# Kernel tuning notes

Hardware: AMD Instinct MI355X
Metric: run time of the kernel (lower is better)

## Reference

```python
import jax, jax.numpy as jnp
import numpy as np

HIDDEN = 32
N_STEPS = 64  # fixed-step RK4 replaces adaptive Dopri5 (same MLP-eval structure)
STD = 0.1     # init_params: Linear weights ~ N(0, 0.1), biases = 0


def _mlp(w1, b1, w2, b2, w3, b3, y):
    # NODE.forward: fc1 -> relu -> fc2 -> relu -> fc3 (t is unused in the source)
    h = jax.nn.relu(y @ w1 + b1)
    h = jax.nn.relu(h @ w2 + b2)
    return h @ w3 + b3


def setup_inputs() -> dict:
    key = jax.random.key(0)
    ks = jax.random.split(key, 8)
    B, D = 131072, 3
    x = jax.random.normal(ks[0], (B, D), dtype=jnp.float32)
    # eval times in (0.1, 1.0], sorted like a posterior-sample schedule
    samples = jnp.sort(
        jax.random.uniform(ks[1], (8, 1), jnp.float32, 0.1, 1.0), axis=0)
    w1 = (STD * jax.random.normal(ks[2], (D, HIDDEN))).astype(jnp.float32)
    b1 = jnp.zeros((HIDDEN,), jnp.float32)
    w2 = (STD * jax.random.normal(ks[3], (HIDDEN, HIDDEN))).astype(jnp.float32)
    b2 = jnp.zeros((HIDDEN,), jnp.float32)
    w3 = (STD * jax.random.normal(ks[4], (HIDDEN, D))).astype(jnp.float32)
    b3 = jnp.zeros((D,), jnp.float32)
    w_out = (STD * jax.random.normal(ks[5], (D, 1))).astype(jnp.float32)
    b_out = jnp.zeros((1,), jnp.float32)
    return {"x": x, "samples": samples, "w1": w1, "b1": b1, "w2": w2,
            "b2": b2, "w3": w3, "b3": b3, "w_out": w_out, "b_out": b_out}


def reference(x, samples, w1, b1, w2, b2, w3, b3, w_out, b_out):
    t_eval = samples[:, 0]                     # (S,)
    max_T = jnp.max(t_eval)
    dt = max_T / N_STEPS

    def step(y, _):
        k1 = _mlp(w1, b1, w2, b2, w3, b3, y)
        k2 = _mlp(w1, b1, w2, b2, w3, b3, y + 0.5 * dt * k1)
        k3 = _mlp(w1, b1, w2, b2, w3, b3, y + 0.5 * dt * k2)
        k4 = _mlp(w1, b1, w2, b2, w3, b3, y + dt * k3)
        y_new = y + (dt / 6.0) * (k1 + 2.0 * k2 + 2.0 * k3 + k4)
        return y_new, y_new

    # traj[i] is the state at time (i+1)*dt; shape (N_STEPS, B, 3)
    _, traj = jax.lax.scan(jax.checkpoint(step), x, jnp.arange(N_STEPS))

    # gather states at the grid step nearest each eval time
    idx = jnp.clip(jnp.round(t_eval / dt).astype(jnp.int32) - 1, 0, N_STEPS - 1)
    y_eval = traj[idx]                         # (S, B, 3)

    # fc_layers readout -> act_vec (S, B, 1)
    return y_eval @ w_out + b_out
```

## Files before the change

kernel.cpp:

```cpp
#include <hip/hip_runtime.h>

#define NSTEPS 64

typedef __attribute__((ext_vector_type(16))) float float16_;
typedef __attribute__((ext_vector_type(2))) __fp16 half2_;
typedef __attribute__((ext_vector_type(8))) __fp16 half8_;

__device__ __forceinline__ half2_ relu_pk_f16(float a, float b) {
    half2_ h = __builtin_amdgcn_cvt_pkrtz(a, b);
    return __builtin_elementwise_max(h, (half2_)(__fp16)0);
}

__global__ __launch_bounds__(256, 4)
void ode_rk4_mfma(const float* __restrict__ x,
                  const float* __restrict__ samples,
                  const float* __restrict__ w1, const float* __restrict__ b1,
                  const float* __restrict__ w2, const float* __restrict__ b2,
                  const float* __restrict__ w3, const float* __restrict__ b3,
                  const float* __restrict__ w_out, const float* __restrict__ b_out,
                  float* __restrict__ out, int B)
{
    const int lane  = threadIdx.x & 63;
    const int w     = threadIdx.x >> 6;
    const int col32 = lane & 31;
    const int half  = lane >> 5;

    const int rowBase = (blockIdx.x * 4 + w) * 32;
    const int row = rowBase + col32;

    auto pi = [](int m) -> int {
        int bb = (m >> 2) & 3;
        return m + ((bb == 1) ? 4 : (bb == 2) ? -4 : 0);
    };

    union { half2_ h2[4]; half8_ h8; } A1;
    {
        int pm = pi(col32);
        if (half == 0) {
            A1.h2[0] = (half2_){(__fp16)w1[0 * 32 + pm], (__fp16)w1[1 * 32 + pm]};
            A1.h2[1] = (half2_){(__fp16)w1[2 * 32 + pm], (__fp16)b1[pm]};
        } else {
            A1.h2[0] = (half2_)(__fp16)0.0f;
            A1.h2[1] = (half2_)(__fp16)0.0f;
        }
        A1.h2[2] = (half2_)(__fp16)0.0f;
        A1.h2[3] = (half2_)(__fp16)0.0f;
    }

    union { half2_ h2[4]; half8_ h8; } W2T1, W2T2;
#pragma unroll
    for (int pp = 0; pp < 4; ++pp) {
        int i1 = half * 8 + 2 * pp;
        W2T1.h2[pp] = (half2_){(__fp16)w2[i1 * 32 + col32], (__fp16)w2[(i1 + 1) * 32 + col32]};
        W2T2.h2[pp] = (half2_){(__fp16)w2[(i1 + 16) * 32 + col32], (__fp16)w2[(i1 + 17) * 32 + col32]};
    }
    float16_ Cb;
#pragma unroll
    for (int r = 0; r < 16; ++r)
        Cb[r] = b2[(r & 3) + 8 * (r >> 2) + 4 * half];

    union { half2_ h2[4]; half8_ h8; } A31, A32;
    {
        const bool live = (col32 < 8) && ((col32 & 3) < 3);
        const int  d    = col32 & 3;
#pragma unroll
        for (int pp = 0; pp < 4; ++pp) {
            int j0 = 2 * pp;
            int nu0 = 4 * half + (j0 & 3) + 8 * (j0 >> 2);
            if (live) {
                A31.h2[pp] = (half2_){(__fp16)w3[nu0 * 3 + d], (__fp16)w3[(nu0 + 1) * 3 + d]};
                A32.h2[pp] = (half2_){(__fp16)w3[(nu0 + 16) * 3 + d], (__fp16)w3[(nu0 + 17) * 3 + d]};
            } else {
                A31.h2[pp] = (half2_)(__fp16)0.0f;
                A32.h2[pp] = (half2_)(__fp16)0.0f;
            }
        }
    }

    float16_ Zc;
#pragma unroll
    for (int r = 0; r < 16; ++r) Zc[r] = 0.0f;

    const float maxT = samples[7];
    const float dt   = maxT / 64.0f;
    const float dt2  = 0.5f * dt;
    const float dt6  = dt / 6.0f;

    int sidx[8];
    unsigned long long smask = 0ull;
#pragma unroll
    for (int j = 0; j < 8; ++j) {
        int id = (int)rintf(samples[j] / dt) - 1;
        id = id < 0 ? 0 : (id > NSTEPS - 1 ? NSTEPS - 1 : id);
        id = __builtin_amdgcn_readfirstlane(id);
        sidx[j] = id;
        smask |= 1ull << id;
    }
    const float wo0 = w_out[0], wo1 = w_out[1], wo2 = w_out[2];
    const float bo  = b_out[0];
    const float b30 = b3[0], b31 = b3[1], b32 = b3[2];

    float y0 = x[(size_t)row * 3 + 0];
    float y1 = x[(size_t)row * 3 + 1];
    float y2 = x[(size_t)row * 3 + 2];

#pragma unroll 1
    for (int s = 0; s < NSTEPS; ++s) {
        float acc0 = 0.f, acc1 = 0.f, acc2 = 0.f;
        float a0 = y0, a1 = y1, a2 = y2;

#pragma unroll
        for (int st = 0; st < 4; ++st) {
            half2_ a01 = __builtin_amdgcn_cvt_pkrtz(a0, a1);
            half2_ a2o = __builtin_amdgcn_cvt_pkrtz(a2, 1.0f);
            union { half2_ h2[4]; half8_ h8; } BL1;
            BL1.h2[0] = a01; BL1.h2[1] = a2o;
            BL1.h2[2] = a01; BL1.h2[3] = a2o;

            float16_ D1 = __builtin_amdgcn_mfma_f32_32x32x16_f16(A1.h8, BL1.h8, Zc, 0, 0, 0);

            union { half2_ h2[4]; half8_ h8; } B1, B2;
#pragma unroll
            for (int pp = 0; pp < 4; ++pp) {
                B1.h2[pp] = relu_pk_f16(D1[2 * pp], D1[2 * pp + 1]);
                B2.h2[pp] = relu_pk_f16(D1[8 + 2 * pp], D1[8 + 2 * pp + 1]);
            }

            float16_ D2a = __builtin_amdgcn_mfma_f32_32x32x16_f16(W2T1.h8, B1.h8, Cb, 0, 0, 0);
            float16_ D2b = __builtin_amdgcn_mfma_f32_32x32x16_f16(W2T2.h8, B2.h8, Zc, 0, 0, 0);

            union { half2_ h2[4]; half8_ h8; } H1, H2;
#pragma unroll
            for (int pp = 0; pp < 4; ++pp) {
                H1.h2[pp] = relu_pk_f16(D2a[2 * pp] + D2b[2 * pp],
                                        D2a[2 * pp + 1] + D2b[2 * pp + 1]);
                H2.h2[pp] = relu_pk_f16(D2a[8 + 2 * pp] + D2b[8 + 2 * pp],
                                        D2a[8 + 2 * pp + 1] + D2b[8 + 2 * pp + 1]);
            }

            float16_ D3a = __builtin_amdgcn_mfma_f32_32x32x16_f16(A31.h8, H1.h8, Zc, 0, 0, 0);
            float16_ D3b = __builtin_amdgcn_mfma_f32_32x32x16_f16(A32.h8, H2.h8, Zc, 0, 0, 0);

            float k0 = D3a[0] + D3b[0] + b30;
            float k1 = D3a[1] + D3b[1] + b31;
            float k2 = D3a[2] + D3b[2] + b32;

            const float ca = (st == 1 || st == 2) ? 2.0f : 1.0f;
            acc0 = fmaf(ca, k0, acc0); acc1 = fmaf(ca, k1, acc1); acc2 = fmaf(ca, k2, acc2);
            const float ci = (st == 2) ? dt : dt2;
            a0 = fmaf(ci, k0, y0); a1 = fmaf(ci, k1, y1); a2 = fmaf(ci, k2, y2);
        }
        y0 = fmaf(dt6, acc0, y0); y1 = fmaf(dt6, acc1, y1); y2 = fmaf(dt6, acc2, y2);

        if ((smask >> s) & 1ull) {
            if (half == 0) {
#pragma unroll
                for (int j = 0; j < 8; ++j) {
                    if (sidx[j] == s) {
                        out[(size_t)j * B + row] = fmaf(y2, wo2, fmaf(y1, wo1, fmaf(y0, wo0, bo)));
                    }
                }
            }
        }
    }
}

extern "C" void kernel_launch(void* const* d_in, const int* in_sizes, int n_in,
                              void* d_out, int out_size, void* d_ws, size_t ws_size,
                              hipStream_t stream) {
    const float* x       = (const float*)d_in[0];
    const float* samples = (const float*)d_in[1];
    const float* w1      = (const float*)d_in[2];
    const float* b1      = (const float*)d_in[3];
    const float* w2      = (const float*)d_in[4];
    const float* b2      = (const float*)d_in[5];
    const float* w3      = (const float*)d_in[6];
    const float* b3      = (const float*)d_in[7];
    const float* w_out   = (const float*)d_in[8];
    const float* b_out   = (const float*)d_in[9];
    float* out = (float*)d_out;

    const int B = in_sizes[0] / 3;
    const int rowsPerBlock = 128;
    const int grid = (B + rowsPerBlock - 1) / rowsPerBlock;
    ode_rk4_mfma<<<grid, 256, 0, stream>>>(
        x, samples, w1, b1, w2, b2, w3, b3, w_out, b_out, out, B);
}
```

Baseline: 227.2 us.

## Fold fc3 into fc1 and carry RK4 state in hidden pre-activation space

Uses linearity to compose W3 with W1 into a 32x32 matrix, so each RK stage needs only the fc2 MMAs plus one fused fc1 update, and the 3-dim state is never rebuilt inside the step. The layer-2 activations are summed in fp16 (SSl/SSh), and the output state is rebuilt only at sample steps via W3 plus a closed-form bias term. This cuts per-step MFMA and conversion work. In exchange, accumulating the trajectory in fp16 over 64 steps risks drift and precision loss.

Result: faster. 207.2 us (-8.8%).

```diff
diff --git a/kernel.cpp b/kernel.cpp
--- a/kernel.cpp
+++ b/kernel.cpp
@@ -3,15 +3,15 @@
 #define NSTEPS 64
 
 typedef __attribute__((ext_vector_type(16))) float float16_;
-typedef __attribute__((ext_vector_type(2))) __fp16 half2_;
-typedef __attribute__((ext_vector_type(8))) __fp16 half8_;
+typedef __attribute__((ext_vector_type(2)))  __fp16 half2_;
+typedef __attribute__((ext_vector_type(8)))  __fp16 half8_;
 
 __device__ __forceinline__ half2_ relu_pk_f16(float a, float b) {
     half2_ h = __builtin_amdgcn_cvt_pkrtz(a, b);
     return __builtin_elementwise_max(h, (half2_)(__fp16)0);
 }
 
-__global__ __launch_bounds__(256, 4)
+__global__ __launch_bounds__(256, 3)
 void ode_rk4_mfma(const float* __restrict__ x,
                   const float* __restrict__ samples,
                   const float* __restrict__ w1, const float* __restrict__ b1,
@@ -25,66 +25,70 @@
     const int col32 = lane & 31;
     const int half  = lane >> 5;
 
-    const int rowBase = (blockIdx.x * 4 + w) * 32;
-    const int row = rowBase + col32;
-
-    auto pi = [](int m) -> int {
-        int bb = (m >> 2) & 3;
-        return m + ((bb == 1) ? 4 : (bb == 2) ? -4 : 0);
+    const int row = (blockIdx.x * 4 + w) * 32 + col32;
+
+    auto nu = [](int k) -> int {
+        return 16 * (k >> 4) + 4 * ((k >> 3) & 1) + (k & 3) + 8 * (((k & 7)) >> 2);
     };
-
-    union { half2_ h2[4]; half8_ h8; } A1;
-    {
-        int pm = pi(col32);
-        if (half == 0) {
-            A1.h2[0] = (half2_){(__fp16)w1[0 * 32 + pm], (__fp16)w1[1 * 32 + pm]};
-            A1.h2[1] = (half2_){(__fp16)w1[2 * 32 + pm], (__fp16)b1[pm]};
-        } else {
-            A1.h2[0] = (half2_)(__fp16)0.0f;
-            A1.h2[1] = (half2_)(__fp16)0.0f;
-        }
-        A1.h2[2] = (half2_)(__fp16)0.0f;
-        A1.h2[3] = (half2_)(__fp16)0.0f;
-    }
-
-    union { half2_ h2[4]; half8_ h8; } W2T1, W2T2;
-#pragma unroll
-    for (int pp = 0; pp < 4; ++pp) {
-        int i1 = half * 8 + 2 * pp;
-        W2T1.h2[pp] = (half2_){(__fp16)w2[i1 * 32 + col32], (__fp16)w2[(i1 + 1) * 32 + col32]};
-        W2T2.h2[pp] = (half2_){(__fp16)w2[(i1 + 16) * 32 + col32], (__fp16)w2[(i1 + 17) * 32 + col32]};
-    }
-    float16_ Cb;
-#pragma unroll
-    for (int r = 0; r < 16; ++r)
-        Cb[r] = b2[(r & 3) + 8 * (r >> 2) + 4 * half];
-
-    union { half2_ h2[4]; half8_ h8; } A31, A32;
-    {
-        const bool live = (col32 < 8) && ((col32 & 3) < 3);
-        const int  d    = col32 & 3;
-#pragma unroll
-        for (int pp = 0; pp < 4; ++pp) {
-            int j0 = 2 * pp;
-            int nu0 = 4 * half + (j0 & 3) + 8 * (j0 >> 2);
-            if (live) {
-                A31.h2[pp] = (half2_){(__fp16)w3[nu0 * 3 + d], (__fp16)w3[(nu0 + 1) * 3 + d]};
-                A32.h2[pp] = (half2_){(__fp16)w3[(nu0 + 16) * 3 + d], (__fp16)w3[(nu0 + 17) * 3 + d]};
-            } else {
-                A31.h2[pp] = (half2_)(__fp16)0.0f;
-                A32.h2[pp] = (half2_)(__fp16)0.0f;
-            }
-        }
-    }
-
-    float16_ Zc;
-#pragma unroll
-    for (int r = 0; r < 16; ++r) Zc[r] = 0.0f;
+    auto rpos = [&](int t) -> int { return (t & 3) + 8 * (t >> 2) + 4 * half; };
 
     const float maxT = samples[7];
     const float dt   = maxT / 64.0f;
     const float dt2  = 0.5f * dt;
     const float dt6  = dt / 6.0f;
+
+    union F { half2_ h2[4]; half8_ h8; };
+
+    F Mh1, Mh2, Mz1, Mz2;
+#pragma unroll
+    for (int pp = 0; pp < 4; ++pp) {
+        int j0 = 2 * pp;
+        int iA = nu(8 * half + j0),      iB = nu(8 * half + j0 + 1);
+        int iC = nu(16 + 8 * half + j0), iD = nu(16 + 8 * half + j0 + 1);
+        float mA = w3[iA * 3 + 0] * w1[0 * 32 + col32] + w3[iA * 3 + 1] * w1[1 * 32 + col32] + w3[iA * 3 + 2] * w1[2 * 32 + col32];
+        float mB = w3[iB * 3 + 0] * w1[0 * 32 + col32] + w3[iB * 3 + 1] * w1[1 * 32 + col32] + w3[iB * 3 + 2] * w1[2 * 32 + col32];
+        float mC = w3[iC * 3 + 0] * w1[0 * 32 + col32] + w3[iC * 3 + 1] * w1[1 * 32 + col32] + w3[iC * 3 + 2] * w1[2 * 32 + col32];
+        float mD = w3[iD * 3 + 0] * w1[0 * 32 + col32] + w3[iD * 3 + 1] * w1[1 * 32 + col32] + w3[iD * 3 + 2] * w1[2 * 32 + col32];
+        Mh1.h2[pp] = (half2_){(__fp16)(dt2 * mA), (__fp16)(dt2 * mB)};
+        Mh2.h2[pp] = (half2_){(__fp16)(dt2 * mC), (__fp16)(dt2 * mD)};
+        Mz1.h2[pp] = (half2_){(__fp16)(dt6 * mA), (__fp16)(dt6 * mB)};
+        Mz2.h2[pp] = (half2_){(__fp16)(dt6 * mC), (__fp16)(dt6 * mD)};
+    }
+
+    F W2T1, W2T2;
+#pragma unroll
+    for (int pp = 0; pp < 4; ++pp) {
+        int j0 = 2 * pp;
+        int iA = nu(8 * half + j0),      iB = nu(8 * half + j0 + 1);
+        int iC = nu(16 + 8 * half + j0), iD = nu(16 + 8 * half + j0 + 1);
+        W2T1.h2[pp] = (half2_){(__fp16)w2[iA * 32 + col32], (__fp16)w2[iB * 32 + col32]};
+        W2T2.h2[pp] = (half2_){(__fp16)w2[iC * 32 + col32], (__fp16)w2[iD * 32 + col32]};
+    }
+    float16_ Cb;
+#pragma unroll
+    for (int r = 0; r < 16; ++r)
+        Cb[r] = b2[rpos(r)];
+
+    F A31, A32;
+    {
+        const int  d    = col32 & 3;
+        const bool live = (col32 < 8) && (d < 3);
+#pragma unroll
+        for (int pp = 0; pp < 4; ++pp) {
+            int j0 = 2 * pp;
+            int iA = nu(8 * half + j0),      iB = nu(8 * half + j0 + 1);
+            int iC = nu(16 + 8 * half + j0), iD = nu(16 + 8 * half + j0 + 1);
+            A31.h2[pp] = live ? (half2_){(__fp16)w3[iA * 3 + d], (__fp16)w3[iB * 3 + d]} : (half2_)(__fp16)0.0f;
+            A32.h2[pp] = live ? (half2_){(__fp16)w3[iC * 3 + d], (__fp16)w3[iD * 3 + d]} : (half2_)(__fp16)0.0f;
+        }
+    }
+
+    float16_ cH;
+#pragma unroll
+    for (int r = 0; r < 16; ++r) {
+        int u = rpos(r);
+        cH[r] = dt2 * (b3[0] * w1[0 * 32 + u] + b3[1] * w1[1 * 32 + u] + b3[2] * w1[2 * 32 + u]);
+    }
 
     int sidx[8];
     unsigned long long smask = 0ull;
@@ -98,66 +102,142 @@
     }
     const float wo0 = w_out[0], wo1 = w_out[1], wo2 = w_out[2];
     const float bo  = b_out[0];
-    const float b30 = b3[0], b31 = b3[1], b32 = b3[2];
-
-    float y0 = x[(size_t)row * 3 + 0];
-    float y1 = x[(size_t)row * 3 + 1];
-    float y2 = x[(size_t)row * 3 + 2];
+    const float db0 = dt * b3[0], db1 = dt * b3[1], db2 = dt * b3[2];
+
+    const float y00 = x[(size_t)row * 3 + 0];
+    const float y01 = x[(size_t)row * 3 + 1];
+    const float y02 = x[(size_t)row * 3 + 2];
+
+    float16_ zb;
+    {
+        F A1y;
+        if (half == 0) {
+            A1y.h2[0] = (half2_){(__fp16)w1[0 * 32 + col32], (__fp16)w1[1 * 32 + col32]};
+            A1y.h2[1] = (half2_){(__fp16)w1[2 * 32 + col32], (__fp16)b1[col32]};
+            A1y.h2[2] = (half2_)(__fp16)0.0f;
+            A1y.h2[3] = (half2_)(__fp16)0.0f;
+        } else {
+#pragma unroll
+            for (int pp = 0; pp < 4; ++pp) A1y.h2[pp] = (half2_)(__fp16)0.0f;
+        }
+        float16_ Zc;
+#pragma unroll
+        for (int r = 0; r < 16; ++r) Zc[r] = 0.0f;
+        half2_ a = __builtin_amdgcn_cvt_pkrtz(y00, y01);
+        half2_ b = __builtin_amdgcn_cvt_pkrtz(y02, 1.0f);
+        F By;
+        By.h2[0] = a; By.h2[1] = b; By.h2[2] = a; By.h2[3] = b;
+        zb = __builtin_amdgcn_mfma_f32_32x32x16_f16(A1y.h8, By.h8, Zc, 0, 0, 0);
+    }
+
+    const half2_ two = (half2_)(__fp16)2.0f;
+    F SSl, SSh;
+#pragma unroll
+    for (int pp = 0; pp < 4; ++pp) { SSl.h2[pp] = (half2_)(__fp16)0.0f; SSh.h2[pp] = (half2_)(__fp16)0.0f; }
 
 #pragma unroll 1
     for (int s = 0; s < NSTEPS; ++s) {
-        float acc0 = 0.f, acc1 = 0.f, acc2 = 0.f;
-        float a0 = y0, a1 = y1, a2 = y2;
-
-#pragma unroll
-        for (int st = 0; st < 4; ++st) {
-            half2_ a01 = __builtin_amdgcn_cvt_pkrtz(a0, a1);
-            half2_ a2o = __builtin_amdgcn_cvt_pkrtz(a2, 1.0f);
-            union { half2_ h2[4]; half8_ h8; } BL1;
-            BL1.h2[0] = a01; BL1.h2[1] = a2o;
-            BL1.h2[2] = a01; BL1.h2[3] = a2o;
-
-            float16_ D1 = __builtin_amdgcn_mfma_f32_32x32x16_f16(A1.h8, BL1.h8, Zc, 0, 0, 0);
-
-            union { half2_ h2[4]; half8_ h8; } B1, B2;
-#pragma unroll
-            for (int pp = 0; pp < 4; ++pp) {
-                B1.h2[pp] = relu_pk_f16(D1[2 * pp], D1[2 * pp + 1]);
-                B2.h2[pp] = relu_pk_f16(D1[8 + 2 * pp], D1[8 + 2 * pp + 1]);
-            }
-
-            float16_ D2a = __builtin_amdgcn_mfma_f32_32x32x16_f16(W2T1.h8, B1.h8, Cb, 0, 0, 0);
-            float16_ D2b = __builtin_amdgcn_mfma_f32_32x32x16_f16(W2T2.h8, B2.h8, Zc, 0, 0, 0);
-
-            union { half2_ h2[4]; half8_ h8; } H1, H2;
-#pragma unroll
-            for (int pp = 0; pp < 4; ++pp) {
-                H1.h2[pp] = relu_pk_f16(D2a[2 * pp] + D2b[2 * pp],
-                                        D2a[2 * pp + 1] + D2b[2 * pp + 1]);
-                H2.h2[pp] = relu_pk_f16(D2a[8 + 2 * pp] + D2b[8 + 2 * pp],
-                                        D2a[8 + 2 * pp + 1] + D2b[8 + 2 * pp + 1]);
-            }
-
-            float16_ D3a = __builtin_amdgcn_mfma_f32_32x32x16_f16(A31.h8, H1.h8, Zc, 0, 0, 0);
-            float16_ D3b = __builtin_amdgcn_mfma_f32_32x32x16_f16(A32.h8, H2.h8, Zc, 0, 0, 0);
-
-            float k0 = D3a[0] + D3b[0] + b30;
-            float k1 = D3a[1] + D3b[1] + b31;
-            float k2 = D3a[2] + D3b[2] + b32;
-
-            const float ca = (st == 1 || st == 2) ? 2.0f : 1.0f;
-            acc0 = fmaf(ca, k0, acc0); acc1 = fmaf(ca, k1, acc1); acc2 = fmaf(ca, k2, acc2);
-            const float ci = (st == 2) ? dt : dt2;
-            a0 = fmaf(ci, k0, y0); a1 = fmaf(ci, k1, y1); a2 = fmaf(ci, k2, y2);
-        }
-        y0 = fmaf(dt6, acc0, y0); y1 = fmaf(dt6, acc1, y1); y2 = fmaf(dt6, acc2, y2);
+        F Pl, Ph, Ql, Qh, Sl, Sh;
+
+#pragma unroll
+        for (int pp = 0; pp < 4; ++pp) {
+            Pl.h2[pp] = relu_pk_f16(zb[2 * pp],     zb[2 * pp + 1]);
+            Ph.h2[pp] = relu_pk_f16(zb[8 + 2 * pp], zb[8 + 2 * pp + 1]);
+        }
+        float16_ D2 = __builtin_amdgcn_mfma_f32_32x32x16_f16(W2T2.h8, Ph.h8,
+                      __builtin_amdgcn_mfma_f32_32x32x16_f16(W2T1.h8, Pl.h8, Cb, 0, 0, 0), 0, 0, 0);
+#pragma unroll
+        for (int pp = 0; pp < 4; ++pp) {
+            Sl.h2[pp] = relu_pk_f16(D2[2 * pp],     D2[2 * pp + 1]);
+            Sh.h2[pp] = relu_pk_f16(D2[8 + 2 * pp], D2[8 + 2 * pp + 1]);
+        }
+
+        float16_ zh = zb + cH;
+
+        {
+            float16_ G = __builtin_amdgcn_mfma_f32_32x32x16_f16(Mh2.h8, Sh.h8,
+                         __builtin_amdgcn_mfma_f32_32x32x16_f16(Mh1.h8, Sl.h8, zh, 0, 0, 0), 0, 0, 0);
+#pragma unroll
+            for (int pp = 0; pp < 4; ++pp) {
+                Pl.h2[pp] = relu_pk_f16(G[2 * pp],     G[2 * pp + 1]);
+                Ph.h2[pp] = relu_pk_f16(G[8 + 2 * pp], G[8 + 2 * pp + 1]);
+            }
+            float16_ E = __builtin_amdgcn_mfma_f32_32x32x16_f16(W2T2.h8, Ph.h8,
+                         __builtin_amdgcn_mfma_f32_32x32x16_f16(W2T1.h8, Pl.h8, Cb, 0, 0, 0), 0, 0, 0);
+#pragma unroll
+            for (int pp = 0; pp < 4; ++pp) {
+                Ql.h2[pp] = relu_pk_f16(E[2 * pp],     E[2 * pp + 1]);
+                Qh.h2[pp] = relu_pk_f16(E[8 + 2 * pp], E[8 + 2 * pp + 1]);
+                Sl.h2[pp] += two * Ql.h2[pp];
+                Sh.h2[pp] += two * Qh.h2[pp];
+            }
+        }
+
+        {
+            float16_ G = __builtin_amdgcn_mfma_f32_32x32x16_f16(Mh2.h8, Qh.h8,
+                         __builtin_amdgcn_mfma_f32_32x32x16_f16(Mh1.h8, Ql.h8, zh, 0, 0, 0), 0, 0, 0);
+#pragma unroll
+            for (int pp = 0; pp < 4; ++pp) {
+                Pl.h2[pp] = relu_pk_f16(G[2 * pp],     G[2 * pp + 1]);
+                Ph.h2[pp] = relu_pk_f16(G[8 + 2 * pp], G[8 + 2 * pp + 1]);
+            }
+            float16_ E = __builtin_amdgcn_mfma_f32_32x32x16_f16(W2T2.h8, Ph.h8,
+                         __builtin_amdgcn_mfma_f32_32x32x16_f16(W2T1.h8, Pl.h8, Cb, 0, 0, 0), 0, 0, 0);
+#pragma unroll
+            for (int pp = 0; pp < 4; ++pp) {
+                Ql.h2[pp] = relu_pk_f16(E[2 * pp],     E[2 * pp + 1]);
+                Qh.h2[pp] = relu_pk_f16(E[8 + 2 * pp], E[8 + 2 * pp + 1]);
+                Sl.h2[pp] += two * Ql.h2[pp];
+                Sh.h2[pp] += two * Qh.h2[pp];
+            }
+        }
+
+        zh = zh + cH;
+        {
+            F Qdl, Qdh;
+#pragma unroll
+            for (int pp = 0; pp < 4; ++pp) {
+                Qdl.h2[pp] = Ql.h2[pp] + Ql.h2[pp];
+                Qdh.h2[pp] = Qh.h2[pp] + Qh.h2[pp];
+            }
+            float16_ G = __builtin_amdgcn_mfma_f32_32x32x16_f16(Mh2.h8, Qdh.h8,
+                         __builtin_amdgcn_mfma_f32_32x32x16_f16(Mh1.h8, Qdl.h8, zh, 0, 0, 0), 0, 0, 0);
+#pragma unroll
+            for (int pp = 0; pp < 4; ++pp) {
+                Pl.h2[pp] = relu_pk_f16(G[2 * pp],     G[2 * pp + 1]);
+                Ph.h2[pp] = relu_pk_f16(G[8 + 2 * pp], G[8 + 2 * pp + 1]);
+            }
+            float16_ E = __builtin_amdgcn_mfma_f32_32x32x16_f16(W2T2.h8, Ph.h8,
+                         __builtin_amdgcn_mfma_f32_32x32x16_f16(W2T1.h8, Pl.h8, Cb, 0, 0, 0), 0, 0, 0);
+#pragma unroll
+            for (int pp = 0; pp < 4; ++pp) {
+                Ql.h2[pp] = relu_pk_f16(E[2 * pp],     E[2 * pp + 1]);
+                Qh.h2[pp] = relu_pk_f16(E[8 + 2 * pp], E[8 + 2 * pp + 1]);
+                Sl.h2[pp] += Ql.h2[pp];
+                Sh.h2[pp] += Qh.h2[pp];
+            }
+        }
+
+#pragma unroll
+        for (int pp = 0; pp < 4; ++pp) { SSl.h2[pp] += Sl.h2[pp]; SSh.h2[pp] += Sh.h2[pp]; }
+        zb = __builtin_amdgcn_mfma_f32_32x32x16_f16(Mz2.h8, Sh.h8,
+             __builtin_amdgcn_mfma_f32_32x32x16_f16(Mz1.h8, Sl.h8, zh, 0, 0, 0), 0, 0, 0);
 
         if ((smask >> s) & 1ull) {
+            float16_ Zc;
+#pragma unroll
+            for (int r = 0; r < 16; ++r) Zc[r] = 0.0f;
+            float16_ D3 = __builtin_amdgcn_mfma_f32_32x32x16_f16(A32.h8, SSh.h8,
+                          __builtin_amdgcn_mfma_f32_32x32x16_f16(A31.h8, SSl.h8, Zc, 0, 0, 0), 0, 0, 0);
+            float T = (float)(s + 1);
+            float o0 = fmaf(dt6, D3[0], fmaf(T, db0, y00));
+            float o1 = fmaf(dt6, D3[1], fmaf(T, db1, y01));
+            float o2 = fmaf(dt6, D3[2], fmaf(T, db2, y02));
             if (half == 0) {
 #pragma unroll
                 for (int j = 0; j < 8; ++j) {
                     if (sidx[j] == s) {
-                        out[(size_t)j * B + row] = fmaf(y2, wo2, fmaf(y1, wo1, fmaf(y0, wo0, bo)));
+                        out[(size_t)j * B + row] = fmaf(o2, wo2, fmaf(o1, wo1, fmaf(o0, wo0, bo)));
                     }
                 }
             }
```
